# Kernel optimization log

Hardware: AMD Instinct MI355X
Metric: run time of the kernel (lower is better)

## Reference

```python
import jax, jax.numpy as jnp
import numpy as np

NUM_OPS = 8
D = 1024
B = 8192


def setup_inputs() -> dict:
    key = jax.random.key(0)
    k1, k2, k3, k4 = jax.random.split(key, 4)
    x = jax.random.normal(k1, (B, D), dtype=jnp.float32)
    logits = 0.001 * jax.random.normal(k2, (NUM_OPS,), dtype=jnp.float32)
    Ws = jax.random.normal(k3, (NUM_OPS, D, D), dtype=jnp.float32) * (1.0 / np.sqrt(D))
    bs = jax.random.normal(k4, (NUM_OPS, D), dtype=jnp.float32) * 0.01
    return {"x": x, "logits": logits, "Ws": Ws, "bs": bs, "num_on_samples": 2}


def reference(x, logits, Ws, bs, num_on_samples):
    # non_stochastic_call: top-k op selection by architecture logits,
    # dispatch x to the selected ops, sum-combine the results.
    _, top_k_ids = jax.lax.top_k(logits, num_on_samples)  # [k]
    W_sel = jnp.take(Ws, top_k_ids, axis=0)  # [k, D, D]
    b_sel = jnp.take(bs, top_k_ids, axis=0)  # [k, D]
    # each op is Dense(D->D) + relu: [k, B, D]
    op_results = jax.nn.relu(jnp.einsum('bd,kde->kbe', x, W_sel) + b_sel[:, None, :])
    return jnp.sum(op_results, axis=0)  # [B, D]
```

## Files before the change

### kernel.cpp

```cpp
#include <hip/hip_runtime.h>
#include <hip/hip_bf16.h>

#define NUM_OPS 8
#define D 1024
#define B_ROWS 8192

typedef unsigned short ushort_t;
typedef __attribute__((ext_vector_type(8))) short bf16x8;
typedef __attribute__((ext_vector_type(4))) float f32x4;
typedef __attribute__((ext_vector_type(4))) float float4v;
typedef __attribute__((ext_vector_type(8))) unsigned short ushort8;

__device__ __forceinline__ unsigned short f2bf(float f) {
    union { float f; unsigned int u; } v; v.f = f;
    unsigned int u = v.u;
    unsigned int lsb = (u >> 16) & 1u;
    u += 0x7fffu + lsb;
    return (unsigned short)(u >> 16);
}

__device__ __forceinline__ void load_lds16(const void* g, void* l) {
    __builtin_amdgcn_global_load_lds(
        (const __attribute__((address_space(1))) void*)g,
        (__attribute__((address_space(3))) void*)l,
        16, 0, 0);
}

__global__ void topk_kernel(const float* __restrict__ logits, int* __restrict__ idx) {
    if (threadIdx.x == 0 && blockIdx.x == 0) {
        float best = -__builtin_inff(); int bi = 0;
        for (int i = 0; i < NUM_OPS; ++i) {
            float v = logits[i];
            if (v > best) { best = v; bi = i; }
        }
        float best2 = -__builtin_inff(); int bi2 = 0;
        for (int i = 0; i < NUM_OPS; ++i) {
            if (i == bi) continue;
            float v = logits[i];
            if (v > best2) { best2 = v; bi2 = i; }
        }
        idx[0] = bi; idx[1] = bi2;
    }
}

__global__ void convert_x(const float* __restrict__ x, ushort_t* __restrict__ xb) {
    int i = (blockIdx.x * 256 + threadIdx.x) * 8;
    float4v v0 = *(const float4v*)(x + i);
    float4v v1 = *(const float4v*)(x + i + 4);
    ushort8 o;
    o[0] = f2bf(v0[0]); o[1] = f2bf(v0[1]); o[2] = f2bf(v0[2]); o[3] = f2bf(v0[3]);
    o[4] = f2bf(v1[0]); o[5] = f2bf(v1[1]); o[6] = f2bf(v1[2]); o[7] = f2bf(v1[3]);
    *(ushort8*)(xb + i) = o;
}

__global__ void gather_transpose_W(const float* __restrict__ Ws,
                                   const int* __restrict__ idx,
                                   ushort_t* __restrict__ Wt) {
    __shared__ float t[32][33];
    int e    = blockIdx.x >> 10;
    int tile = blockIdx.x & 1023;
    int td = (tile >> 5) << 5;
    int te = (tile & 31) << 5;
    int tx = threadIdx.x & 31, ty = threadIdx.x >> 5;
    const float* W = Ws + (size_t)idx[e] * D * D;
    for (int r = 0; r < 4; ++r)
        t[ty + 8 * r][tx] = W[(size_t)(td + ty + 8 * r) * D + te + tx];
    __syncthreads();
    ushort_t* o = Wt + (size_t)e * D * D;
    for (int r = 0; r < 4; ++r)
        o[(size_t)(te + ty + 8 * r) * D + td + tx] = f2bf(t[tx][ty + 8 * r]);
}

__device__ __forceinline__ void stage_half_A(const ushort_t* __restrict__ Abf,
                                             int brow, int t, ushort_t* dstbuf,
                                             int h, int tid, int wv) {
    #pragma unroll
    for (int i = 0; i < 2; ++i) {
        const int c   = i * 512 + tid;
        const int rr  = c >> 3;
        const int cb  = (c & 7) * 16;
        const int gcb = cb ^ ((rr & 7) << 4);
        const ushort_t* g = Abf + (size_t)(brow + h * 128 + rr) * D + t * 64 + (gcb >> 1);
        ushort_t* l = dstbuf + (h * 16384 + (i * 512 + wv * 64) * 16) / 2;
        load_lds16(g, l);
    }
}

__device__ __forceinline__ void stage_half_B(const ushort_t* __restrict__ Wt,
                                             int bcolIdx, int t, ushort_t* dstbuf,
                                             int h, int tid, int wv) {
    #pragma unroll
    for (int i = 0; i < 2; ++i) {
        const int c   = i * 512 + tid;
        const int rr  = c >> 3;
        const int cb  = (c & 7) * 16;
        const int gcb = cb ^ ((rr & 7) << 4);
        const ushort_t* g = Wt + (size_t)h * D * D
                          + (size_t)(bcolIdx * 128 + rr) * D + t * 64 + (gcb >> 1);
        ushort_t* l = dstbuf + (h * 16384 + (i * 512 + wv * 64) * 16) / 2;
        load_lds16(g, l);
    }
}

#define BAR()   do { __builtin_amdgcn_s_barrier(); __builtin_amdgcn_sched_barrier(0); } while (0)
#define LGKM0() do { asm volatile("s_waitcnt lgkmcnt(0)" ::: "memory"); __builtin_amdgcn_sched_barrier(0); } while (0)
#define VM(N)   do { asm volatile("s_waitcnt vmcnt(" #N ")" ::: "memory"); __builtin_amdgcn_sched_barrier(0); } while (0)
#define PRIO1() __builtin_amdgcn_s_setprio(1)
#define PRIO0() __builtin_amdgcn_s_setprio(0)

#define DS_A(mh)                                                                   \
    do {                                                                           \
        _Pragma("unroll") for (int kk = 0; kk < 2; ++kk)                           \
        _Pragma("unroll") for (int m = 0; m < 4; ++m)                              \
            af[kk][m] = *(const bf16x8*)(curA +                                    \
                (size_t)((wr * 128 + (mh) * 64 + m * 16 + l15) * 128) +            \
                (kk ? x1 : x0));                                                   \
    } while (0)

#define DS_B(E)                                                                    \
    do {                                                                           \
        _Pragma("unroll") for (int kk = 0; kk < 2; ++kk)                           \
        _Pragma("unroll") for (int n = 0; n < 2; ++n)                              \
            bfr[E][kk][n] = *(const bf16x8*)(curB +                                \
                (size_t)(((E) * 128 + wc * 32 + n * 16 + l15) * 128) +             \
                (kk ? x1 : x0));                                                   \
    } while (0)

#define MM(E, mh)                                                                  \
    do {                                                                           \
        _Pragma("unroll") for (int kk = 0; kk < 2; ++kk)                           \
        _Pragma("unroll") for (int m = 0; m < 4; ++m)                              \
        _Pragma("unroll") for (int n = 0; n < 2; ++n)                              \
            acc[E][(mh) * 4 + m][n] = __builtin_amdgcn_mfma_f32_16x16x32_bf16(     \
                af[kk][m], bfr[E][kk][n], acc[E][(mh) * 4 + m][n], 0, 0, 0);       \
    } while (0)

__global__ __launch_bounds__(512, 2)
void gemm_dual(const ushort_t* __restrict__ Abf, const ushort_t* __restrict__ Wt,
               const float* __restrict__ bs, const int* __restrict__ idx,
               float* __restrict__ out) {
    constexpr int NT = D / 64;
    __shared__ __align__(16) ushort_t ldsA[2][256 * 64];
    __shared__ __align__(16) ushort_t ldsB[2][256 * 64];

    const int tid  = threadIdx.x;
    const int wv   = tid >> 6;
    const int lane = tid & 63;
    const int wr   = wv >> 2, wc = wv & 3;
    const int l15  = lane & 15, lq = lane >> 4;
    const int swz  = (lane & 7) << 4;
    const int x0   = (lq * 16) ^ swz;
    const int x1   = (64 + lq * 16) ^ swz;

    const int bid     = blockIdx.x;
    const int brow    = (bid >> 3) * 256;
    const int bcolIdx = bid & 7;

    f32x4  acc[2][8][2] = {};
    bf16x8 af[2][4];
    bf16x8 bfr[2][2][2];

    stage_half_A(Abf, brow, 0, ldsA[0], 0, tid, wv);
    stage_half_A(Abf, brow, 0, ldsA[0], 1, tid, wv);
    stage_half_B(Wt, bcolIdx, 0, ldsB[0], 0, tid, wv);
    stage_half_B(Wt, bcolIdx, 0, ldsB[0], 1, tid, wv);
    VM(0);
    BAR();

    for (int t = 0; t < NT - 1; ++t) {
        const char* curA = (const char*)ldsA[t & 1];
        const char* curB = (const char*)ldsB[t & 1];
        ushort_t* nA = ldsA[(t & 1) ^ 1];
        ushort_t* nB = ldsB[(t & 1) ^ 1];

        DS_A(0); DS_B(0);
        stage_half_A(Abf, brow, t + 1, nA, 0, tid, wv);
        BAR(); LGKM0();
        PRIO1(); MM(0, 0); PRIO0();
        VM(2);
        BAR();

        DS_B(1);
        stage_half_A(Abf, brow, t + 1, nA, 1, tid, wv);
        BAR(); LGKM0();
        PRIO1(); MM(1, 0); PRIO0();
        BAR();

        DS_A(1);
        stage_half_B(Wt, bcolIdx, t + 1, nB, 0, tid, wv);
        BAR(); LGKM0();
        PRIO1(); MM(1, 1); PRIO0();
        BAR();

        stage_half_B(Wt, bcolIdx, t + 1, nB, 1, tid, wv);
        BAR(); LGKM0();
        PRIO1(); MM(0, 1); PRIO0();
        VM(2);
        BAR();
    }

    {
        const char* curA = (const char*)ldsA[(NT - 1) & 1];
        const char* curB = (const char*)ldsB[(NT - 1) & 1];

        DS_A(0); DS_B(0);
        BAR(); LGKM0();
        PRIO1(); MM(0, 0); PRIO0();
        VM(0);
        BAR();

        DS_B(1);
        BAR(); LGKM0();
        PRIO1(); MM(1, 0); PRIO0();
        BAR();

        DS_A(1);
        BAR(); LGKM0();
        PRIO1(); MM(1, 1); PRIO0();
        BAR();

        LGKM0();
        PRIO1(); MM(0, 1); PRIO0();
    }

    const int i0 = idx[0], i1 = idx[1];
    #pragma unroll
    for (int n = 0; n < 2; ++n) {
        const int col = bcolIdx * 128 + wc * 32 + n * 16 + l15;
        const float b0 = bs[i0 * D + col];
        const float b1 = bs[i1 * D + col];
        #pragma unroll
        for (int m = 0; m < 8; ++m) {
            const int rbase = brow + wr * 128 + m * 16 + lq * 4;
            #pragma unroll
            for (int i = 0; i < 4; ++i) {
                float v0 = acc[0][m][n][i] + b0; v0 = v0 > 0.f ? v0 : 0.f;
                float v1 = acc[1][m][n][i] + b1; v1 = v1 > 0.f ? v1 : 0.f;
                out[(size_t)(rbase + i) * D + col] = v0 + v1;
            }
        }
    }
}

extern "C" void kernel_launch(void* const* d_in, const int* in_sizes, int n_in,
                              void* d_out, int out_size, void* d_ws, size_t ws_size,
                              hipStream_t stream) {
    const float* x      = (const float*)d_in[0];
    const float* logits = (const float*)d_in[1];
    const float* Ws     = (const float*)d_in[2];
    const float* bs     = (const float*)d_in[3];
    float* out = (float*)d_out;

    char* ws = (char*)d_ws;
    ushort_t* xbf = (ushort_t*)ws;
    ushort_t* Wt  = (ushort_t*)(ws + (size_t)B_ROWS * D * 2);
    int* idx      = (int*)(ws + (size_t)B_ROWS * D * 2 + (size_t)2 * D * D * 2);

    topk_kernel<<<1, 1, 0, stream>>>(logits, idx);
    convert_x<<<(B_ROWS * D) / (256 * 8), 256, 0, stream>>>(x, xbf);
    gather_transpose_W<<<2 * (D / 32) * (D / 32), 256, 0, stream>>>(Ws, idx, Wt);

    gemm_dual<<<256, 512, 0, stream>>>(xbf, Wt, bs, idx, out);
}
```

Measured before the change: 58.66 us.

## Deepen prefetch pipeline to stage half-tiles two iterations ahead

```diff
diff --git a/kernel.cpp b/kernel.cpp
--- a/kernel.cpp
+++ b/kernel.cpp
@@ -113,7 +113,7 @@
         _Pragma("unroll") for (int kk = 0; kk < 2; ++kk)                           \
         _Pragma("unroll") for (int m = 0; m < 4; ++m)                              \
             af[kk][m] = *(const bf16x8*)(curA +                                    \
-                (size_t)((wr * 128 + (mh) * 64 + m * 16 + l15) * 128) +            \
+                (size_t)(((mh) * 128 + wr * 64 + m * 16 + l15) * 128) +            \
                 (kk ? x1 : x0));                                                   \
     } while (0)
 
@@ -161,52 +161,50 @@
     bf16x8 bfr[2][2][2];
 
     stage_half_A(Abf, brow, 0, ldsA[0], 0, tid, wv);
-    stage_half_A(Abf, brow, 0, ldsA[0], 1, tid, wv);
     stage_half_B(Wt, bcolIdx, 0, ldsB[0], 0, tid, wv);
     stage_half_B(Wt, bcolIdx, 0, ldsB[0], 1, tid, wv);
-    VM(0);
+    stage_half_A(Abf, brow, 0, ldsA[0], 1, tid, wv);
+    stage_half_A(Abf, brow, 1, ldsA[1], 0, tid, wv);
+    stage_half_B(Wt, bcolIdx, 1, ldsB[1], 1, tid, wv);
+    VM(8);
     BAR();
 
-    for (int t = 0; t < NT - 1; ++t) {
-        const char* curA = (const char*)ldsA[t & 1];
-        const char* curB = (const char*)ldsB[t & 1];
-        ushort_t* nA = ldsA[(t & 1) ^ 1];
-        ushort_t* nB = ldsB[(t & 1) ^ 1];
+    for (int u = 0; u < NT - 1; ++u) {
+        const char* curA = (const char*)ldsA[u & 1];
+        const char* curB = (const char*)ldsB[u & 1];
 
         DS_A(0); DS_B(0);
-        stage_half_A(Abf, brow, t + 1, nA, 0, tid, wv);
+        if (u + 1 < NT) stage_half_B(Wt, bcolIdx, u + 1, ldsB[(u + 1) & 1], 0, tid, wv);
         BAR(); LGKM0();
         PRIO1(); MM(0, 0); PRIO0();
-        VM(2);
-        BAR();
+        VM(6); BAR();
 
         DS_B(1);
-        stage_half_A(Abf, brow, t + 1, nA, 1, tid, wv);
+        if (u + 1 < NT) stage_half_A(Abf, brow, u + 1, ldsA[(u + 1) & 1], 1, tid, wv);
         BAR(); LGKM0();
         PRIO1(); MM(1, 0); PRIO0();
-        BAR();
+        VM(6); BAR();
 
         DS_A(1);
-        stage_half_B(Wt, bcolIdx, t + 1, nB, 0, tid, wv);
+        if (u + 2 < NT) stage_half_A(Abf, brow, u + 2, ldsA[u & 1], 0, tid, wv);
         BAR(); LGKM0();
         PRIO1(); MM(1, 1); PRIO0();
-        BAR();
-
-        stage_half_B(Wt, bcolIdx, t + 1, nB, 1, tid, wv);
+        VM(6); BAR();
+
+        if (u + 2 < NT) stage_half_B(Wt, bcolIdx, u + 2, ldsB[u & 1], 1, tid, wv);
         BAR(); LGKM0();
         PRIO1(); MM(0, 1); PRIO0();
-        VM(2);
-        BAR();
+        VM(6); BAR();
     }
 
     {
         const char* curA = (const char*)ldsA[(NT - 1) & 1];
         const char* curB = (const char*)ldsB[(NT - 1) & 1];
+        VM(0); BAR();
 
         DS_A(0); DS_B(0);
         BAR(); LGKM0();
         PRIO1(); MM(0, 0); PRIO0();
-        VM(0);
         BAR();
 
         DS_B(1);
@@ -230,12 +228,14 @@
         const float b0 = bs[i0 * D + col];
         const float b1 = bs[i1 * D + col];
         #pragma unroll
-        for (int m = 0; m < 8; ++m) {
-            const int rbase = brow + wr * 128 + m * 16 + lq * 4;
+        for (int mh = 0; mh < 2; ++mh)
+        #pragma unroll
+        for (int m = 0; m < 4; ++m) {
+            const int rbase = brow + mh * 128 + wr * 64 + m * 16 + lq * 4;
             #pragma unroll
             for (int i = 0; i < 4; ++i) {
-                float v0 = acc[0][m][n][i] + b0; v0 = v0 > 0.f ? v0 : 0.f;
-                float v1 = acc[1][m][n][i] + b1; v1 = v1 > 0.f ? v1 : 0.f;
+                float v0 = acc[0][mh * 4 + m][n][i] + b0; v0 = v0 > 0.f ? v0 : 0.f;
+                float v1 = acc[1][mh * 4 + m][n][i] + b1; v1 = v1 > 0.f ? v1 : 0.f;
                 out[(size_t)(rbase + i) * D + col] = v0 + v1;
             }
         }
```

Measured after the change: 58.27 us. Within noise of the previous version (-0.7%).
